# Kernel optimization log

Measured on AMD Instinct MI355X. Metric: run time of the kernel, lower is better.

## Reference

```python
import jax, jax.numpy as jnp
import numpy as np

COMMITMENT_COST = 0.25

def setup_inputs() -> dict:
    key = jax.random.key(0)
    k1, k2 = jax.random.split(key)
    inputs = jax.random.normal(k1, (16, 256, 64, 64), dtype=jnp.float32)   # [B, C=D, H, W]
    embedding = jax.random.normal(k2, (2048, 256), dtype=jnp.float32)      # [K, D] codebook
    return {"inputs": inputs, "embedding": embedding}

def reference(inputs, embedding):
    K, D = embedding.shape
    x = jnp.transpose(inputs, (0, 2, 3, 1))            # [B, H, W, D]
    flat = x.reshape(-1, D)                            # [N, D]
    distances = (jnp.sum(flat * flat, axis=1, keepdims=True)
                 + jnp.sum(embedding * embedding, axis=1)
                 - 2.0 * flat @ embedding.T)
    idx = jnp.argmin(distances, axis=1)                # [N]
    encodings = jax.nn.one_hot(idx, K, dtype=flat.dtype)  # [N, K]
    quantized = embedding[idx].reshape(x.shape)        # gather == one_hot @ embedding
    # commitment loss (eval mode: only e_latent term, scaled)
    e_latent_loss = jnp.mean((jax.lax.stop_gradient(quantized) - x) ** 2)
    loss = COMMITMENT_COST * e_latent_loss
    # straight-through estimator
    quantized_st = x + jax.lax.stop_gradient(quantized - x)
    avg_probs = jnp.mean(encodings, axis=0)
    perplexity = jnp.exp(-jnp.sum(avg_probs * jnp.log(avg_probs + 1e-10)))
    return (loss,
            jnp.transpose(quantized_st, (0, 3, 1, 2)),  # back to [B, C, H, W]
            perplexity,
            encodings)
```

## Files before the change

kernel.cpp:

```cpp
#include <hip/hip_runtime.h>

#define KCODES  2048
#define DDIM    256

#define OUT_LOSS 0
#define OUT_Q    1
#define OUT_PERP 16777217
#define OUT_ENC  16777218

#define WS_E2   1048576
#define WS_CNT  1056768
#define WS_SUM  1064960
#define WS_EHI  2097152

typedef _Float16 f16x8 __attribute__((ext_vector_type(8)));
typedef _Float16 f16x4 __attribute__((ext_vector_type(4)));
typedef float    f32x4 __attribute__((ext_vector_type(4)));
typedef float    f32x2 __attribute__((ext_vector_type(2)));

__device__ __forceinline__ void gld16(const void* g, void* l) {
    __builtin_amdgcn_global_load_lds((const __attribute__((address_space(1))) void*)g,
                                     (__attribute__((address_space(3))) void*)l, 16, 0, 0);
}

#define MERGE2(m1,i1,m2,i2,n1,j1,n2,j2)                                   \
    {                                                                     \
        const bool w_ = ((n1) < (m1)) || ((n1) == (m1) && (j1) < (i1));   \
        const float w1_ = w_ ? (n1) : (m1); const int wi_ = w_ ? (j1) : (i1); \
        const float l1_ = w_ ? (m1) : (n1); const int li_ = w_ ? (i1) : (j1); \
        const float c2_ = w_ ? (n2) : (m2); const int ci_ = w_ ? (j2) : (i2); \
        const bool s_ = ((c2_) < (l1_)) || ((c2_) == (l1_) && (ci_) < (li_)); \
        (m1) = w1_; (i1) = wi_;                                           \
        (m2) = s_ ? c2_ : l1_; (i2) = s_ ? ci_ : li_;                     \
    }

__launch_bounds__(256)
__global__ void k_e2split(const float* __restrict__ emb, _Float16* __restrict__ Ehi,
                          float* __restrict__ e2, int* __restrict__ counts,
                          float* __restrict__ sumsq) {
    const int wave = threadIdx.x >> 6;
    const int lane = threadIdx.x & 63;
    const int k = blockIdx.x * 4 + wave;
    const float4 v = *(const float4*)(emb + k * DDIM + lane * 4);
    f16x4 h;
    h[0] = (_Float16)v.x; h[1] = (_Float16)v.y; h[2] = (_Float16)v.z; h[3] = (_Float16)v.w;
    *(f16x4*)(Ehi + k * DDIM + lane * 4) = h;
    float s = v.x * v.x + v.y * v.y + v.z * v.z + v.w * v.w;
#pragma unroll
    for (int off = 32; off >= 1; off >>= 1) s += __shfl_down(s, off);
    if (lane == 0) e2[k] = s;
    if (blockIdx.x < 8) counts[blockIdx.x * 256 + threadIdx.x] = 0;
    if (blockIdx.x == 8 && threadIdx.x == 0) sumsq[0] = 0.0f;
}

__launch_bounds__(256, 2)
__global__ void k_main(const float* __restrict__ inp, const float* __restrict__ emb,
                       const _Float16* __restrict__ Ehi, const float* __restrict__ e2g,
                       int* __restrict__ counts, float* __restrict__ sumsq,
                       float* __restrict__ outQ, float* __restrict__ encQ) {
    __shared__ __align__(16) char pool[81920];
    _Float16* A  = (_Float16*)pool;
    _Float16* Bh = (_Float16*)(pool + 65536);

    const int rb  = blockIdx.x;
    const int b   = rb >> 5;
    const int hw0 = (rb & 31) << 7;
    const int n0  = rb << 7;
    const int tid = threadIdx.x;
    const int w = tid >> 6, lane = tid & 63;
    const int lq = lane >> 4, lm = lane & 15;
    const int wr = (w >> 1) * 64, wc = (w & 1) * 64;
    const int r8 = lane >> 3, c8 = lane & 7;
    const int gch = c8 ^ r8;

    const float* base = inp + (size_t)b * 1048576 + hw0;
#pragma unroll 4
    for (int rr = 0; rr < 16; ++rr) {
        const int row = ((rr & 1) << 6) + lane;
        const int cg  = ((rr >> 1) << 2) + w;
        const float* p = base + (size_t)(cg << 3) * 4096 + row;
        float v[8];
#pragma unroll
        for (int j = 0; j < 8; ++j) v[j] = p[(size_t)j * 4096];
        f16x8 h;
#pragma unroll
        for (int j = 0; j < 8; ++j) h[j] = (_Float16)v[j];
        const int q  = cg >> 3;
        const int ch = cg & 7;
        *(f16x8*)&A[row * 256 + q * 64 + ((ch ^ (row & 7)) << 3)] = h;
    }
    __syncthreads();

    const int sw0 = ((lq    ) ^ (lm & 7)) << 3;
    const int sw1 = ((lq ^ 4) ^ (lm & 7)) << 3;

    float V1[4][4], V2[4][4]; int I1[4][4], I2[4][4];
#pragma unroll
    for (int i = 0; i < 4; ++i)
#pragma unroll
        for (int rr = 0; rr < 4; ++rr) {
            V1[i][rr] = 3.402823466e38f; V2[i][rr] = 3.402823466e38f;
            I1[i][rr] = 0x7fffffff;      I2[i][rr] = 0x7fffffff;
        }

#pragma unroll 1
    for (int ct = 0; ct < 16; ++ct) {
        const int c0 = ct * 128;
        float e2v[4];
#pragma unroll
        for (int j = 0; j < 4; ++j) e2v[j] = e2g[c0 + wc + j * 16 + lm];

        f32x4 acc[4][4];
#pragma unroll
        for (int i = 0; i < 4; ++i)
#pragma unroll
            for (int j = 0; j < 4; ++j) acc[i][j] = (f32x4)(0.0f);

#pragma unroll 1
        for (int kt = 0; kt < 4; ++kt) {
            const int d0 = kt * 64;
            __syncthreads();
#pragma unroll
            for (int i = 0; i < 4; ++i) {
                const int Row = i * 32 + w * 8 + r8;
                gld16(Ehi + (size_t)(c0 + Row) * DDIM + d0 + gch * 8, &Bh[(i * 32 + w * 8) * 64]);
            }
            __syncthreads();
#pragma unroll
            for (int s = 0; s < 2; ++s) {
                const int wch = s * 4 + lq;
                const int sw = s ? sw1 : sw0;
                f16x8 af[4], bf[4];
#pragma unroll
                for (int t = 0; t < 4; ++t) {
                    const int Rb = wc + t * 16 + lm;
                    af[t] = *(const f16x8*)&A[(wr + t * 16 + lm) * 256 + d0 + sw];
                    bf[t] = *(const f16x8*)&Bh[Rb * 64 + ((wch ^ (Rb & 7)) << 3)];
                }
#pragma unroll
                for (int i = 0; i < 4; ++i)
#pragma unroll
                    for (int j = 0; j < 4; ++j)
                        acc[i][j] = __builtin_amdgcn_mfma_f32_16x16x32_f16(af[i], bf[j], acc[i][j], 0, 0, 0);
            }
        }

#pragma unroll
        for (int i = 0; i < 4; ++i)
#pragma unroll
            for (int j = 0; j < 4; ++j) {
                const int idx = c0 + wc + j * 16 + lm;
#pragma unroll
                for (int rr = 0; rr < 4; ++rr) {
                    const float dist = fmaf(-2.0f, acc[i][j][rr], e2v[j]);
                    const bool b1 = dist < V1[i][rr];
                    const bool b2 = dist < V2[i][rr];
                    V2[i][rr] = b1 ? V1[i][rr] : (b2 ? dist : V2[i][rr]);
                    I2[i][rr] = b1 ? I1[i][rr] : (b2 ? idx  : I2[i][rr]);
                    V1[i][rr] = b1 ? dist : V1[i][rr];
                    I1[i][rr] = b1 ? idx  : I1[i][rr];
                }
            }
    }

    __syncthreads();
    float4* red  = (float4*)pool;
    int*    idxs = (int*)(pool + 4096);
    float*  lsum = (float*)(pool + 4608);
    float*  xf   = (float*)(pool + 8192);
#pragma unroll
    for (int i = 0; i < 4; ++i)
#pragma unroll
        for (int rr = 0; rr < 4; ++rr) {
            float m1 = V1[i][rr]; int i1 = I1[i][rr];
            float m2 = V2[i][rr]; int i2 = I2[i][rr];
#pragma unroll
            for (int off = 1; off < 16; off <<= 1) {
                const float n1 = __shfl_xor(m1, off); const int j1 = __shfl_xor(i1, off);
                const float n2 = __shfl_xor(m2, off); const int j2 = __shfl_xor(i2, off);
                MERGE2(m1, i1, m2, i2, n1, j1, n2, j2);
            }
            if (lm == 0) {
                const int row = wr + i * 16 + lq * 4 + rr;
                red[row * 2 + (w & 1)] = make_float4(m1, __int_as_float(i1),
                                                     m2, __int_as_float(i2));
            }
        }
    if (tid == 0) *lsum = 0.f;

    const int g16 = tid >> 4;
    float Sp[8][4], X2r[8];
#pragma unroll
    for (int rr = 0; rr < 8; ++rr) {
        X2r[rr] = 0.f;
#pragma unroll
        for (int c = 0; c < 4; ++c) Sp[rr][c] = 0.f;
    }

#pragma unroll 1
    for (int h = 0; h < 2; ++h) {
        __syncthreads();
#pragma unroll 8
        for (int k2 = 0; k2 < 32; ++k2) {
            const int dloc = w * 32 + k2;
            const float* sp = base + (size_t)(h * 128 + dloc) * 4096;
            xf[dloc * 129 + lane]      = sp[lane];
            xf[dloc * 129 + 64 + lane] = sp[64 + lane];
        }
        __syncthreads();
#pragma unroll
        for (int rr = 0; rr < 8; ++rr) {
            const int r = g16 * 8 + rr;
            const float4 Ac = red[r * 2];
            const float4 Bc = red[r * 2 + 1];
            const int cid[4] = {__float_as_int(Ac.y), __float_as_int(Ac.w),
                                __float_as_int(Bc.y), __float_as_int(Bc.w)};
            float x8[8];
#pragma unroll
            for (int j = 0; j < 8; ++j) x8[j] = xf[(lm * 8 + j) * 129 + r];
#pragma unroll
            for (int j = 0; j < 8; ++j) X2r[rr] = fmaf(x8[j], x8[j], X2r[rr]);
#pragma unroll
            for (int c = 0; c < 4; ++c) {
                const float* ep = emb + (size_t)cid[c] * DDIM + h * 128 + lm * 8;
                const float4 e0 = *(const float4*)ep;
                const float4 e1 = *(const float4*)(ep + 4);
                float s = Sp[rr][c];
                s = fmaf(x8[0], e0.x, s); s = fmaf(x8[1], e0.y, s);
                s = fmaf(x8[2], e0.z, s); s = fmaf(x8[3], e0.w, s);
                s = fmaf(x8[4], e1.x, s); s = fmaf(x8[5], e1.y, s);
                s = fmaf(x8[6], e1.z, s); s = fmaf(x8[7], e1.w, s);
                Sp[rr][c] = s;
            }
        }
    }

    float lracc = 0.f;
#pragma unroll
    for (int rr = 0; rr < 8; ++rr) {
        const int r = g16 * 8 + rr;
        float s0 = Sp[rr][0], s1 = Sp[rr][1], s2 = Sp[rr][2], s3 = Sp[rr][3];
        float x2v = X2r[rr];
#pragma unroll
        for (int off = 1; off < 16; off <<= 1) {
            s0 += __shfl_xor(s0, off); s1 += __shfl_xor(s1, off);
            s2 += __shfl_xor(s2, off); s3 += __shfl_xor(s3, off);
            x2v += __shfl_xor(x2v, off);
        }
        const float4 Ac = red[r * 2];
        const float4 Bc = red[r * 2 + 1];
        const int cid[4] = {__float_as_int(Ac.y), __float_as_int(Ac.w),
                            __float_as_int(Bc.y), __float_as_int(Bc.w)};
        const float S4[4] = {s0, s1, s2, s3};
        float bv = 3.402823466e38f; int bi = 0; float sb = 0.f, eb = 0.f;
#pragma unroll
        for (int k = 0; k < 4; ++k) {
            const float ev = e2g[cid[k]];
            const float dv = fmaf(-2.0f, S4[k], ev);
            if (dv < bv || (dv == bv && cid[k] < bi)) { bv = dv; bi = cid[k]; sb = S4[k]; eb = ev; }
        }
        if (lm == rr) {
            idxs[r] = bi;
            atomicAdd(&counts[bi], 1);
            lracc = x2v - 2.0f * sb + eb;
        }
    }
#pragma unroll
    for (int off = 32; off >= 1; off >>= 1) lracc += __shfl_down(lracc, off);
    if (lane == 0) atomicAdd(lsum, lracc);
    __syncthreads();
    if (tid == 0) atomicAdd(sumsq, *lsum);

    f32x2* erow = (f32x2*)encQ + (size_t)n0 * 1024;
#pragma unroll 1
    for (int rr = 0; rr < 128; ++rr) {
        const int id = idxs[rr];
        f32x2* rp = erow + (size_t)rr * 1024;
#pragma unroll
        for (int k = 0; k < 4; ++k) {
            const int c2 = k * 256 + tid;
            const int ccc = c2 * 2;
            f32x2 v;
            v[0] = (ccc == id) ? 1.0f : 0.0f;
            v[1] = (ccc + 1 == id) ? 1.0f : 0.0f;
            __builtin_nontemporal_store(v, rp + c2);
        }
    }

    float* Qs = (float*)(pool + 8192);
    const int gq = tid >> 4, lmq = tid & 15;
#pragma unroll 1
    for (int c = 0; c < 4; ++c) {
        __syncthreads();
#pragma unroll
        for (int rr2 = 0; rr2 < 2; ++rr2) {
            const int rl = gq * 2 + rr2;
            const float* ep = emb + (size_t)idxs[c * 32 + rl] * DDIM + lmq * 16;
#pragma unroll
            for (int j = 0; j < 4; ++j)
                *(float4*)&Qs[rl * 260 + lmq * 16 + j * 4] = *(const float4*)(ep + j * 4);
        }
        __syncthreads();
        float* op = outQ + (size_t)b * 1048576 + hw0 + c * 32;
        const int dh = lane >> 5, hl = lane & 31;
#pragma unroll 8
        for (int dd = 0; dd < 32; ++dd) {
            const int d = w * 64 + dd * 2 + dh;
            __builtin_nontemporal_store(Qs[hl * 260 + d], op + (size_t)d * 4096 + hl);
        }
    }
}

__launch_bounds__(256)
__global__ void k_finalize(const int* __restrict__ counts, const float* __restrict__ sumsq,
                           float* __restrict__ out) {
    __shared__ float red[256];
    const int t = threadIdx.x;
    float s = 0.0f;
    for (int k = t; k < KCODES; k += 256) {
        const float p = (float)counts[k] * (1.0f / 65536.0f);
        s += p * logf(p + 1e-10f);
    }
    red[t] = s;
    __syncthreads();
    for (int off = 128; off >= 1; off >>= 1) {
        if (t < off) red[t] += red[t + off];
        __syncthreads();
    }
    if (t == 0) {
        out[OUT_PERP] = expf(-red[0]);
        out[OUT_LOSS] = 0.25f * sumsq[0] * (1.0f / 16777216.0f);
    }
}

extern "C" void kernel_launch(void* const* d_in, const int* in_sizes, int n_in,
                              void* d_out, int out_size, void* d_ws, size_t ws_size,
                              hipStream_t stream) {
    const float* inp = (const float*)d_in[0];
    const float* emb = (const float*)d_in[1];
    float* out = (float*)d_out;
    char* wsb  = (char*)d_ws;

    float*    e2     = (float*)(wsb + WS_E2);
    int*      counts = (int*)(wsb + WS_CNT);
    float*    sumsq  = (float*)(wsb + WS_SUM);
    _Float16* Ehi    = (_Float16*)(wsb + WS_EHI);

    k_e2split <<<512, 256, 0, stream>>>(emb, Ehi, e2, counts, sumsq);
    k_main    <<<512, 256, 0, stream>>>(inp, emb, Ehi, e2, counts, sumsq,
                                        out + OUT_Q, out + OUT_ENC);
    k_finalize<<<1,   256, 0, stream>>>(counts, sumsq, out);
}
```

Baseline: 854.0 us.

## Halve row tile to 64, double-buffer codebook tiles, launch 1024 blocks

Shrinks each block's row tile from 128 to 64 rows, so the grid doubles to 1024 blocks and shared memory drops to 64 KB. The codebook-tile loads are double-buffered: the next tile is issued before the current one is consumed, and one barrier per step replaces two. The aim is to fill all compute units and hide global-to-LDS load latency behind the MFMA work. The cost is twice as many codebook tile loads overall and a lower MFMA-to-load ratio per wave. The rescoring transpose layout is also changed to allow vectorized reads.

```diff
diff --git a/kernel.cpp b/kernel.cpp
--- a/kernel.cpp
+++ b/kernel.cpp
@@ -58,26 +58,27 @@
                        const _Float16* __restrict__ Ehi, const float* __restrict__ e2g,
                        int* __restrict__ counts, float* __restrict__ sumsq,
                        float* __restrict__ outQ, float* __restrict__ encQ) {
-    __shared__ __align__(16) char pool[81920];
-    _Float16* A  = (_Float16*)pool;
-    _Float16* Bh = (_Float16*)(pool + 65536);
+    __shared__ __align__(16) char pool[65536];
+    _Float16* A   = (_Float16*)pool;
+    _Float16* Bh0 = (_Float16*)(pool + 32768);
+    _Float16* Bh1 = (_Float16*)(pool + 49152);
 
     const int rb  = blockIdx.x;
-    const int b   = rb >> 5;
-    const int hw0 = (rb & 31) << 7;
-    const int n0  = rb << 7;
+    const int b   = rb >> 6;
+    const int hw0 = (rb & 63) << 6;
+    const int n0  = rb << 6;
     const int tid = threadIdx.x;
     const int w = tid >> 6, lane = tid & 63;
     const int lq = lane >> 4, lm = lane & 15;
-    const int wr = (w >> 1) * 64, wc = (w & 1) * 64;
+    const int wr = (w >> 1) * 32, wc = (w & 1) * 64;
     const int r8 = lane >> 3, c8 = lane & 7;
     const int gch = c8 ^ r8;
 
     const float* base = inp + (size_t)b * 1048576 + hw0;
-#pragma unroll 4
-    for (int rr = 0; rr < 16; ++rr) {
-        const int row = ((rr & 1) << 6) + lane;
-        const int cg  = ((rr >> 1) << 2) + w;
+#pragma unroll 2
+    for (int rr = 0; rr < 8; ++rr) {
+        const int row = lane;
+        const int cg  = rr * 4 + w;
         const float* p = base + (size_t)(cg << 3) * 4096 + row;
         float v[8];
 #pragma unroll
@@ -89,87 +90,100 @@
         const int ch = cg & 7;
         *(f16x8*)&A[row * 256 + q * 64 + ((ch ^ (row & 7)) << 3)] = h;
     }
+
+    {
+#pragma unroll
+        for (int i = 0; i < 4; ++i)
+            gld16(Ehi + (size_t)(i * 32 + w * 8 + r8) * DDIM + gch * 8,
+                  Bh0 + (i * 32 + w * 8) * 64);
+    }
     __syncthreads();
 
     const int sw0 = ((lq    ) ^ (lm & 7)) << 3;
     const int sw1 = ((lq ^ 4) ^ (lm & 7)) << 3;
 
-    float V1[4][4], V2[4][4]; int I1[4][4], I2[4][4];
-#pragma unroll
-    for (int i = 0; i < 4; ++i)
+    float V1[2][4], V2[2][4]; int I1[2][4], I2[2][4];
+#pragma unroll
+    for (int i = 0; i < 2; ++i)
 #pragma unroll
         for (int rr = 0; rr < 4; ++rr) {
             V1[i][rr] = 3.402823466e38f; V2[i][rr] = 3.402823466e38f;
             I1[i][rr] = 0x7fffffff;      I2[i][rr] = 0x7fffffff;
         }
 
+    float e2v[4];
+    f32x4 acc[2][4];
 #pragma unroll 1
-    for (int ct = 0; ct < 16; ++ct) {
-        const int c0 = ct * 128;
-        float e2v[4];
-#pragma unroll
-        for (int j = 0; j < 4; ++j) e2v[j] = e2g[c0 + wc + j * 16 + lm];
-
-        f32x4 acc[4][4];
-#pragma unroll
-        for (int i = 0; i < 4; ++i)
-#pragma unroll
-            for (int j = 0; j < 4; ++j) acc[i][j] = (f32x4)(0.0f);
-
-#pragma unroll 1
-        for (int kt = 0; kt < 4; ++kt) {
-            const int d0 = kt * 64;
-            __syncthreads();
-#pragma unroll
-            for (int i = 0; i < 4; ++i) {
-                const int Row = i * 32 + w * 8 + r8;
-                gld16(Ehi + (size_t)(c0 + Row) * DDIM + d0 + gch * 8, &Bh[(i * 32 + w * 8) * 64]);
-            }
-            __syncthreads();
-#pragma unroll
-            for (int s = 0; s < 2; ++s) {
-                const int wch = s * 4 + lq;
-                const int sw = s ? sw1 : sw0;
-                f16x8 af[4], bf[4];
-#pragma unroll
-                for (int t = 0; t < 4; ++t) {
-                    const int Rb = wc + t * 16 + lm;
-                    af[t] = *(const f16x8*)&A[(wr + t * 16 + lm) * 256 + d0 + sw];
-                    bf[t] = *(const f16x8*)&Bh[Rb * 64 + ((wch ^ (Rb & 7)) << 3)];
+    for (int step = 0; step < 64; ++step) {
+        const int ct = step >> 2, kt = step & 3;
+        const int c0 = ct * 128, d0 = kt * 64;
+
+        if (step < 63) {
+            const int ctn = (step + 1) >> 2, ktn = (step + 1) & 3;
+            _Float16* bdst = ((step + 1) & 1) ? Bh1 : Bh0;
+            const size_t soff = (size_t)(ctn * 128) * DDIM + ktn * 64 + gch * 8;
+#pragma unroll
+            for (int i = 0; i < 4; ++i)
+                gld16(Ehi + soff + (size_t)(i * 32 + w * 8 + r8) * DDIM,
+                      bdst + (i * 32 + w * 8) * 64);
+        }
+        if (kt == 0) {
+#pragma unroll
+            for (int j = 0; j < 4; ++j) e2v[j] = e2g[c0 + wc + j * 16 + lm];
+#pragma unroll
+            for (int i = 0; i < 2; ++i)
+#pragma unroll
+                for (int j = 0; j < 4; ++j) acc[i][j] = (f32x4)(0.0f);
+        }
+
+        const _Float16* Bc = (step & 1) ? Bh1 : Bh0;
+#pragma unroll
+        for (int s = 0; s < 2; ++s) {
+            const int wch = s * 4 + lq;
+            const int sw = s ? sw1 : sw0;
+            f16x8 af[2], bf[4];
+#pragma unroll
+            for (int t = 0; t < 2; ++t)
+                af[t] = *(const f16x8*)&A[(wr + t * 16 + lm) * 256 + d0 + sw];
+#pragma unroll
+            for (int t = 0; t < 4; ++t) {
+                const int Rb = wc + t * 16 + lm;
+                bf[t] = *(const f16x8*)&Bc[Rb * 64 + ((wch ^ (Rb & 7)) << 3)];
+            }
+#pragma unroll
+            for (int i = 0; i < 2; ++i)
+#pragma unroll
+                for (int j = 0; j < 4; ++j)
+                    acc[i][j] = __builtin_amdgcn_mfma_f32_16x16x32_f16(af[i], bf[j], acc[i][j], 0, 0, 0);
+        }
+        __syncthreads();
+
+        if (kt == 3) {
+#pragma unroll
+            for (int i = 0; i < 2; ++i)
+#pragma unroll
+                for (int j = 0; j < 4; ++j) {
+                    const int idx = c0 + wc + j * 16 + lm;
+#pragma unroll
+                    for (int rr = 0; rr < 4; ++rr) {
+                        const float dist = fmaf(-2.0f, acc[i][j][rr], e2v[j]);
+                        const bool b1 = dist < V1[i][rr];
+                        const bool b2 = dist < V2[i][rr];
+                        V2[i][rr] = b1 ? V1[i][rr] : (b2 ? dist : V2[i][rr]);
+                        I2[i][rr] = b1 ? I1[i][rr] : (b2 ? idx  : I2[i][rr]);
+                        V1[i][rr] = b1 ? dist : V1[i][rr];
+                        I1[i][rr] = b1 ? idx  : I1[i][rr];
+                    }
                 }
-#pragma unroll
-                for (int i = 0; i < 4; ++i)
-#pragma unroll
-                    for (int j = 0; j < 4; ++j)
-                        acc[i][j] = __builtin_amdgcn_mfma_f32_16x16x32_f16(af[i], bf[j], acc[i][j], 0, 0, 0);
-            }
-        }
-
-#pragma unroll
-        for (int i = 0; i < 4; ++i)
-#pragma unroll
-            for (int j = 0; j < 4; ++j) {
-                const int idx = c0 + wc + j * 16 + lm;
-#pragma unroll
-                for (int rr = 0; rr < 4; ++rr) {
-                    const float dist = fmaf(-2.0f, acc[i][j][rr], e2v[j]);
-                    const bool b1 = dist < V1[i][rr];
-                    const bool b2 = dist < V2[i][rr];
-                    V2[i][rr] = b1 ? V1[i][rr] : (b2 ? dist : V2[i][rr]);
-                    I2[i][rr] = b1 ? I1[i][rr] : (b2 ? idx  : I2[i][rr]);
-                    V1[i][rr] = b1 ? dist : V1[i][rr];
-                    I1[i][rr] = b1 ? idx  : I1[i][rr];
-                }
-            }
-    }
-
-    __syncthreads();
+        }
+    }
+
     float4* red  = (float4*)pool;
-    int*    idxs = (int*)(pool + 4096);
-    float*  lsum = (float*)(pool + 4608);
-    float*  xf   = (float*)(pool + 8192);
-#pragma unroll
-    for (int i = 0; i < 4; ++i)
+    int*    idxs = (int*)(pool + 2048);
+    float*  lsum = (float*)(pool + 2304);
+    float*  xf   = (float*)(pool + 4096);
+#pragma unroll
+    for (int i = 0; i < 2; ++i)
 #pragma unroll
         for (int rr = 0; rr < 4; ++rr) {
             float m1 = V1[i][rr]; int i1 = I1[i][rr];
@@ -189,9 +203,9 @@
     if (tid == 0) *lsum = 0.f;
 
     const int g16 = tid >> 4;
-    float Sp[8][4], X2r[8];
-#pragma unroll
-    for (int rr = 0; rr < 8; ++rr) {
+    float Sp[4][4], X2r[4];
+#pragma unroll
+    for (int rr = 0; rr < 4; ++rr) {
         X2r[rr] = 0.f;
 #pragma unroll
         for (int c = 0; c < 4; ++c) Sp[rr][c] = 0.f;
@@ -204,20 +218,23 @@
         for (int k2 = 0; k2 < 32; ++k2) {
             const int dloc = w * 32 + k2;
             const float* sp = base + (size_t)(h * 128 + dloc) * 4096;
-            xf[dloc * 129 + lane]      = sp[lane];
-            xf[dloc * 129 + 64 + lane] = sp[64 + lane];
-        }
-        __syncthreads();
-#pragma unroll
-        for (int rr = 0; rr < 8; ++rr) {
-            const int r = g16 * 8 + rr;
+            xf[lane * 129 + dloc] = sp[lane];
+        }
+        __syncthreads();
+#pragma unroll
+        for (int rr = 0; rr < 4; ++rr) {
+            const int r = g16 * 4 + rr;
             const float4 Ac = red[r * 2];
-            const float4 Bc = red[r * 2 + 1];
+            const float4 Bc4 = red[r * 2 + 1];
             const int cid[4] = {__float_as_int(Ac.y), __float_as_int(Ac.w),
-                                __float_as_int(Bc.y), __float_as_int(Bc.w)};
+                                __float_as_int(Bc4.y), __float_as_int(Bc4.w)};
             float x8[8];
-#pragma unroll
-            for (int j = 0; j < 8; ++j) x8[j] = xf[(lm * 8 + j) * 129 + r];
+            {
+                const float4 xa = *(const float4*)&xf[r * 129 + lm * 8];
+                const float4 xb = *(const float4*)&xf[r * 129 + lm * 8 + 4];
+                x8[0] = xa.x; x8[1] = xa.y; x8[2] = xa.z; x8[3] = xa.w;
+                x8[4] = xb.x; x8[5] = xb.y; x8[6] = xb.z; x8[7] = xb.w;
+            }
 #pragma unroll
             for (int j = 0; j < 8; ++j) X2r[rr] = fmaf(x8[j], x8[j], X2r[rr]);
 #pragma unroll
@@ -237,8 +254,8 @@
 
     float lracc = 0.f;
 #pragma unroll
-    for (int rr = 0; rr < 8; ++rr) {
-        const int r = g16 * 8 + rr;
+    for (int rr = 0; rr < 4; ++rr) {
+        const int r = g16 * 4 + rr;
         float s0 = Sp[rr][0], s1 = Sp[rr][1], s2 = Sp[rr][2], s3 = Sp[rr][3];
         float x2v = X2r[rr];
 #pragma unroll
@@ -248,9 +265,9 @@
             x2v += __shfl_xor(x2v, off);
         }
         const float4 Ac = red[r * 2];
-        const float4 Bc = red[r * 2 + 1];
+        const float4 Bc4 = red[r * 2 + 1];
         const int cid[4] = {__float_as_int(Ac.y), __float_as_int(Ac.w),
-                            __float_as_int(Bc.y), __float_as_int(Bc.w)};
+                            __float_as_int(Bc4.y), __float_as_int(Bc4.w)};
         const float S4[4] = {s0, s1, s2, s3};
         float bv = 3.402823466e38f; int bi = 0; float sb = 0.f, eb = 0.f;
 #pragma unroll
@@ -273,7 +290,7 @@
 
     f32x2* erow = (f32x2*)encQ + (size_t)n0 * 1024;
 #pragma unroll 1
-    for (int rr = 0; rr < 128; ++rr) {
+    for (int rr = 0; rr < 64; ++rr) {
         const int id = idxs[rr];
         f32x2* rp = erow + (size_t)rr * 1024;
 #pragma unroll
@@ -287,10 +304,10 @@
         }
     }
 
-    float* Qs = (float*)(pool + 8192);
+    float* Qs = (float*)(pool + 4096);
     const int gq = tid >> 4, lmq = tid & 15;
 #pragma unroll 1
-    for (int c = 0; c < 4; ++c) {
+    for (int c = 0; c < 2; ++c) {
         __syncthreads();
 #pragma unroll
         for (int rr2 = 0; rr2 < 2; ++rr2) {
@@ -346,8 +363,8 @@
     float*    sumsq  = (float*)(wsb + WS_SUM);
     _Float16* Ehi    = (_Float16*)(wsb + WS_EHI);
 
-    k_e2split <<<512, 256, 0, stream>>>(emb, Ehi, e2, counts, sumsq);
-    k_main    <<<512, 256, 0, stream>>>(inp, emb, Ehi, e2, counts, sumsq,
-                                        out + OUT_Q, out + OUT_ENC);
-    k_finalize<<<1,   256, 0, stream>>>(counts, sumsq, out);
-}
+    k_e2split <<<512,  256, 0, stream>>>(emb, Ehi, e2, counts, sumsq);
+    k_main    <<<1024, 256, 0, stream>>>(inp, emb, Ehi, e2, counts, sumsq,
+                                         out + OUT_Q, out + OUT_ENC);
+    k_finalize<<<1,    256, 0, stream>>>(counts, sumsq, out);
+}
```

Measured after the change: 835.1 us. 1.02x faster.
